# Performance work log

Hardware: AMD Instinct MI355X
Metric: run time of the kernel (lower is better)

## Reference

```python
import jax, jax.numpy as jnp
import numpy as np

# --- GridEncoder config (matches torch-ngp defaults) ---
D = 3                 # input_dim
L = 16                # num_levels
C = 2                 # level_dim
H = 16                # base_resolution
PLS = 2.0             # per_level_scale
LOG2_HASHMAP = 19
MAX_PARAMS = 2 ** LOG2_HASHMAP
PRIMES = (1, 2654435761, 805459861)  # fast_hash primes for D=3
ALIGN_CORNERS = False


def _level_meta():
    """Replicates the offsets computation in GridEncoder.__init__ and the
    kernel's per-level resolution / hash-vs-dense decision."""
    metas = []
    off = 0
    for l in range(L):
        res = int(np.ceil(H * PLS ** l))            # kernel: ceil(exp2(l*S)*H - 1) + 1 == H*2^l here
        full = (res if ALIGN_CORNERS else res + 1) ** D
        params = min(MAX_PARAMS, full)
        params = int(np.ceil(params / 8) * 8)       # pad to multiple of 8
        hashed = full > params                      # kernel: stride > hashmap_size after index loop
        metas.append((off, params, res, hashed))
        off += params
    return metas, off

METAS, TOTAL_PARAMS = _level_meta()


def setup_inputs() -> dict:
    key = jax.random.key(0)
    k1, k2 = jax.random.split(key)
    B = 1048576
    inputs = jax.random.uniform(k1, (B, D), dtype=jnp.float32, minval=-1.0, maxval=1.0)
    # reset_parameters(): uniform(-1e-4, 1e-4)
    embeddings = jax.random.uniform(k2, (TOTAL_PARAMS, C), dtype=jnp.float32,
                                    minval=-1e-4, maxval=1e-4)
    return {"inputs": inputs, "embeddings": embeddings}


def _grid_encode(x, embeddings):
    """x: [B, D] in [0, 1]. Returns [B, L*C]."""
    corner_bits = jnp.array([[(c >> d) & 1 for d in range(D)] for c in range(2 ** D)],
                            dtype=jnp.uint32)                       # [8, D]
    primes = jnp.array(PRIMES, dtype=jnp.uint32)
    outs = []
    for l, (off, size, res, hashed) in enumerate(METAS):
        scale = float(np.exp2(l) * H - 1.0)                          # exp2(l*S)*H - 1, S = log2(2) = 1
        pos = x * scale + (0.0 if ALIGN_CORNERS else 0.5)            # [B, D]
        pg_f = jnp.floor(pos)
        frac = pos - pg_f                                            # [B, D] linear interp weights
        pg = pg_f.astype(jnp.uint32)                                 # [B, D]
        corners = pg[None, :, :] + corner_bits[:, None, :]           # [8, B, D]
        # N-linear interpolation weights: prod over dims of frac / (1-frac)
        w = jnp.prod(jnp.where(corner_bits[:, None, :] == 1,
                               frac[None, :, :], 1.0 - frac[None, :, :]), axis=-1)  # [8, B]
        if hashed:
            # fast_hash: xor of pos_grid[d] * primes[d] in wrapping uint32
            idx = corners[..., 0] * primes[0]
            for d in range(1, D):
                idx = idx ^ (corners[..., d] * primes[d])
        else:
            base = res if ALIGN_CORNERS else res + 1
            stride = jnp.array([base ** d for d in range(D)], dtype=jnp.uint32)
            idx = (corners * stride).sum(axis=-1).astype(jnp.uint32)
        idx = (idx % jnp.uint32(size)) + jnp.uint32(off)             # [8, B]
        emb = embeddings[idx]                                        # [8, B, C] gather
        outs.append(jnp.einsum('kb,kbc->bc', w, emb))                # [B, C]
    return jnp.concatenate(outs, axis=-1)                            # [B, L*C], level-major


def reference(inputs, embeddings):
    bound = 1.0
    x = (inputs + bound) / (2.0 * bound)   # map to [0, 1]
    return _grid_encode(x, embeddings)
```

## Files before the change

kernel.cpp:

```cpp
#include <hip/hip_runtime.h>
#include <cstdint>


namespace {

using f32x2 = __attribute__((ext_vector_type(2))) float;
using f32x4 = __attribute__((ext_vector_type(4))) float;

__device__ __forceinline__ void level_setup(
    float x, float y, float z, uint32_t l,
    uint32_t idx[8], float w[8]) {
  uint32_t res = 16u << l;
  float scale = (float)res - 1.0f;

  float px = x * scale + 0.5f;
  float py = y * scale + 0.5f;
  float pz = z * scale + 0.5f;
  float gx = floorf(px), gy = floorf(py), gz = floorf(pz);
  float rx = px - gx, ry = py - gy, rz = pz - gz;
  uint32_t ix = (uint32_t)gx, iy = (uint32_t)gy, iz = (uint32_t)gz;

  uint32_t off = (l >= 3u) ? (l * 524288u - 1257368u)
                           : ((l == 0u) ? 0u : ((l == 1u) ? 4920u : 40864u));
  bool hashed = (l >= 3u);

  uint32_t base = res + 1u;
  uint32_t bb = base * base;
  const uint32_t P2 = 2654435761u, P3 = 805459861u;

  uint32_t dy0 = iy * base, dy1 = dy0 + base;
  uint32_t dz0 = iz * bb,   dz1 = dz0 + bb;
  uint32_t hy0 = iy * P2,   hy1 = hy0 + P2;
  uint32_t hz0 = iz * P3,   hz1 = hz0 + P3;

#pragma unroll
  for (int c = 0; c < 8; ++c) {
    uint32_t cx = ix + (uint32_t)(c & 1);
    uint32_t h = (cx ^ ((c & 2) ? hy1 : hy0) ^ ((c & 4) ? hz1 : hz0)) & 0x7FFFFu;
    uint32_t d = cx + ((c & 2) ? dy1 : dy0) + ((c & 4) ? dz1 : dz0);
    idx[c] = (hashed ? h : d) + off;
  }

  float wx1 = rx, wx0 = 1.0f - rx;
  float wy1 = ry, wy0 = 1.0f - ry;
  float wz1 = rz, wz0 = 1.0f - rz;
#pragma unroll
  for (int c = 0; c < 8; ++c) {
    w[c] = ((c & 1) ? wx1 : wx0) *
           ((c & 2) ? wy1 : wy0) *
           ((c & 4) ? wz1 : wz0);
  }
}

__global__ __launch_bounds__(256) void gather_lm_kernel(
    const float* __restrict__ in,
    const f32x2* __restrict__ emb,
    f32x2* __restrict__ ws,
    uint32_t B) {
  uint32_t l = blockIdx.y;
  uint32_t p = blockIdx.x * 256u + threadIdx.x;
  if (p >= B) return;

  float x = (__builtin_nontemporal_load(&in[p * 3 + 0]) + 1.0f) * 0.5f;
  float y = (__builtin_nontemporal_load(&in[p * 3 + 1]) + 1.0f) * 0.5f;
  float z = (__builtin_nontemporal_load(&in[p * 3 + 2]) + 1.0f) * 0.5f;

  uint32_t idx[8];
  float w[8];
  level_setup(x, y, z, l, idx, w);

  f32x2 e[8];
#pragma unroll
  for (int c = 0; c < 8; ++c) e[c] = emb[idx[c]];

  float o0 = 0.0f, o1 = 0.0f;
#pragma unroll
  for (int c = 0; c < 8; ++c) {
    o0 = fmaf(w[c], e[c].x, o0);
    o1 = fmaf(w[c], e[c].y, o1);
  }

  f32x2 r; r.x = o0; r.y = o1;
  __builtin_nontemporal_store(r, &ws[(size_t)l * B + p]);
}

__global__ __launch_bounds__(256) void transpose_kernel(
    const f32x2* __restrict__ ws,
    f32x4* __restrict__ out,
    uint32_t B) {
  __shared__ f32x2 lds[16 * 257];
  uint32_t tid = threadIdx.x;
  uint32_t p0 = blockIdx.x * 256u;

#pragma unroll
  for (uint32_t l = 0; l < 16u; ++l) {
    lds[l * 257u + tid] =
        __builtin_nontemporal_load(&ws[(size_t)l * B + p0 + tid]);
  }
  __syncthreads();

#pragma unroll
  for (uint32_t m = 0; m < 8u; ++m) {
    uint32_t lin = m * 256u + tid;
    uint32_t q = lin >> 3;
    uint32_t j2 = lin & 7u;
    f32x2 a = lds[(2u * j2)      * 257u + q];
    f32x2 b = lds[(2u * j2 + 1u) * 257u + q];
    f32x4 v; v.x = a.x; v.y = a.y; v.z = b.x; v.w = b.y;
    __builtin_nontemporal_store(v, &out[(size_t)p0 * 8u + lin]);
  }
}

__global__ __launch_bounds__(256) void grid_encode_fallback(
    const float* __restrict__ in, const f32x2* __restrict__ emb,
    f32x4* __restrict__ out, uint32_t B) {
  uint32_t p = blockIdx.x * 256u + threadIdx.x;
  if (p >= B) return;
  float x = (in[p * 3 + 0] + 1.0f) * 0.5f;
  float y = (in[p * 3 + 1] + 1.0f) * 0.5f;
  float z = (in[p * 3 + 2] + 1.0f) * 0.5f;
#pragma unroll 1
  for (uint32_t l = 0; l < 16u; l += 2u) {
    uint32_t ia[8], ib[8]; float wa[8], wb[8];
    level_setup(x, y, z, l, ia, wa);
    level_setup(x, y, z, l + 1u, ib, wb);
    f32x2 ea[8], eb[8];
#pragma unroll
    for (int c = 0; c < 8; ++c) ea[c] = emb[ia[c]];
#pragma unroll
    for (int c = 0; c < 8; ++c) eb[c] = emb[ib[c]];
    float a0 = 0, a1 = 0, b0 = 0, b1 = 0;
#pragma unroll
    for (int c = 0; c < 8; ++c) {
      a0 = fmaf(wa[c], ea[c].x, a0);
      a1 = fmaf(wa[c], ea[c].y, a1);
      b0 = fmaf(wb[c], eb[c].x, b0);
      b1 = fmaf(wb[c], eb[c].y, b1);
    }
    f32x4 v; v.x = a0; v.y = a1; v.z = b0; v.w = b1;
    out[(size_t)p * 8u + (l >> 1)] = v;
  }
}

}

extern "C" void kernel_launch(void* const* d_in, const int* in_sizes, int n_in,
                              void* d_out, int out_size, void* d_ws, size_t ws_size,
                              hipStream_t stream) {
  (void)n_in; (void)out_size;
  const float* in = (const float*)d_in[0];
  const f32x2* emb = (const f32x2*)d_in[1];
  f32x4* out = (f32x4*)d_out;
  uint32_t B = (uint32_t)(in_sizes[0] / 3);
  uint32_t pblocks = (B + 255u) / 256u;

  size_t ws_needed = (size_t)16 * B * sizeof(f32x2);
  if (ws_size >= ws_needed) {
    f32x2* ws = (f32x2*)d_ws;
    hipLaunchKernelGGL(gather_lm_kernel, dim3(pblocks, 16), dim3(256), 0,
                       stream, in, emb, ws, B);
    hipLaunchKernelGGL(transpose_kernel, dim3(pblocks), dim3(256), 0,
                       stream, ws, out, B);
  } else {
    hipLaunchKernelGGL(grid_encode_fallback, dim3(pblocks), dim3(256), 0,
                       stream, in, emb, out, B);
  }
}
```

Before: 619.4 us.

## Pair hashed x-neighbour gathers into 16-byte loads and simplify transpose

In the gather kernel, hashed levels with even ix now fetch both x-neighbours with one aligned 16-byte load, because ix^h and (ix+1)^h differ only in the low bit, then pick the halves by parity. Dense and hashed levels are split into separate branches, which avoids computing both index forms. The transpose kernel drops its LDS staging and has each thread read two level-major pairs and write one 16-byte output. This cuts the number of random memory transactions in the gather, but adds branch divergence on ix parity, and the transpose now reads the workspace with a stride pattern that may coalesce less well.

```diff
diff --git a/kernel.cpp b/kernel.cpp
--- a/kernel.cpp
+++ b/kernel.cpp
@@ -65,19 +65,71 @@
   float y = (__builtin_nontemporal_load(&in[p * 3 + 1]) + 1.0f) * 0.5f;
   float z = (__builtin_nontemporal_load(&in[p * 3 + 2]) + 1.0f) * 0.5f;
 
-  uint32_t idx[8];
-  float w[8];
-  level_setup(x, y, z, l, idx, w);
+  uint32_t res = 16u << l;
+  float scale = (float)res - 1.0f;
+  float px = x * scale + 0.5f;
+  float py = y * scale + 0.5f;
+  float pz = z * scale + 0.5f;
+  float gx = floorf(px), gy = floorf(py), gz = floorf(pz);
+  float rx = px - gx, ry = py - gy, rz = pz - gz;
+  uint32_t ix = (uint32_t)gx, iy = (uint32_t)gy, iz = (uint32_t)gz;
 
   f32x2 e[8];
-#pragma unroll
-  for (int c = 0; c < 8; ++c) e[c] = emb[idx[c]];
+
+  if (l >= 3u) {
+    uint32_t off = l * 524288u - 1257368u;
+    const f32x2* __restrict__ tab = emb + off;
+    const uint32_t P2 = 2654435761u, P3 = 805459861u;
+    uint32_t hy0 = iy * P2, hy1 = hy0 + P2;
+    uint32_t hz0 = iz * P3, hz1 = hz0 + P3;
+    uint32_t hb0 = hy0 ^ hz0, hb1 = hy1 ^ hz0, hb2 = hy0 ^ hz1, hb3 = hy1 ^ hz1;
+    uint32_t hb[4] = {hb0, hb1, hb2, hb3};
+
+    if ((ix & 1u) == 0u) {
+#pragma unroll
+      for (int j = 0; j < 4; ++j) {
+        uint32_t h0 = (ix ^ hb[j]) & 0x7FFFFu;
+        f32x4 v = *reinterpret_cast<const f32x4*>(tab + (h0 & ~1u));
+        f32x2 lo; lo.x = v.x; lo.y = v.y;
+        f32x2 hi; hi.x = v.z; hi.y = v.w;
+        bool swap = (h0 & 1u) != 0u;
+        e[2 * j]     = swap ? hi : lo;
+        e[2 * j + 1] = swap ? lo : hi;
+      }
+    } else {
+      uint32_t ix1 = ix + 1u;
+#pragma unroll
+      for (int j = 0; j < 4; ++j) {
+        e[2 * j]     = tab[(ix  ^ hb[j]) & 0x7FFFFu];
+        e[2 * j + 1] = tab[(ix1 ^ hb[j]) & 0x7FFFFu];
+      }
+    }
+  } else {
+    uint32_t off = (l == 0u) ? 0u : ((l == 1u) ? 4920u : 40864u);
+    uint32_t base = res + 1u;
+    uint32_t bb = base * base;
+    uint32_t dy0 = iy * base, dy1 = dy0 + base;
+    uint32_t dz0 = iz * bb,   dz1 = dz0 + bb;
+#pragma unroll
+    for (int c = 0; c < 8; ++c) {
+      uint32_t cx = ix + (uint32_t)(c & 1);
+      uint32_t d = cx + ((c & 2) ? dy1 : dy0) + ((c & 4) ? dz1 : dz0);
+      e[c] = emb[d + off];
+    }
+  }
+
+  float wx1 = rx, wx0 = 1.0f - rx;
+  float wy1 = ry, wy0 = 1.0f - ry;
+  float wz1 = rz, wz0 = 1.0f - rz;
 
   float o0 = 0.0f, o1 = 0.0f;
 #pragma unroll
   for (int c = 0; c < 8; ++c) {
-    o0 = fmaf(w[c], e[c].x, o0);
-    o1 = fmaf(w[c], e[c].y, o1);
+    float w = ((c & 1) ? wx1 : wx0) *
+              ((c & 2) ? wy1 : wy0) *
+              ((c & 4) ? wz1 : wz0);
+    o0 = fmaf(w, e[c].x, o0);
+    o1 = fmaf(w, e[c].y, o1);
   }
 
   f32x2 r; r.x = o0; r.y = o1;
@@ -88,27 +140,14 @@
     const f32x2* __restrict__ ws,
     f32x4* __restrict__ out,
     uint32_t B) {
-  __shared__ f32x2 lds[16 * 257];
-  uint32_t tid = threadIdx.x;
-  uint32_t p0 = blockIdx.x * 256u;
-
-#pragma unroll
-  for (uint32_t l = 0; l < 16u; ++l) {
-    lds[l * 257u + tid] =
-        __builtin_nontemporal_load(&ws[(size_t)l * B + p0 + tid]);
-  }
-  __syncthreads();
-
-#pragma unroll
-  for (uint32_t m = 0; m < 8u; ++m) {
-    uint32_t lin = m * 256u + tid;
-    uint32_t q = lin >> 3;
-    uint32_t j2 = lin & 7u;
-    f32x2 a = lds[(2u * j2)      * 257u + q];
-    f32x2 b = lds[(2u * j2 + 1u) * 257u + q];
-    f32x4 v; v.x = a.x; v.y = a.y; v.z = b.x; v.w = b.y;
-    __builtin_nontemporal_store(v, &out[(size_t)p0 * 8u + lin]);
-  }
+  uint32_t t = blockIdx.x * 256u + threadIdx.x;
+  if (t >= B * 8u) return;
+  uint32_t j = t & 7u;
+  uint32_t q = t >> 3;
+  f32x2 a = __builtin_nontemporal_load(&ws[(size_t)(2u * j)      * B + q]);
+  f32x2 b = __builtin_nontemporal_load(&ws[(size_t)(2u * j + 1u) * B + q]);
+  f32x4 v; v.x = a.x; v.y = a.y; v.z = b.x; v.w = b.y;
+  __builtin_nontemporal_store(v, &out[t]);
 }
 
 __global__ __launch_bounds__(256) void grid_encode_fallback(
@@ -159,7 +198,8 @@
     f32x2* ws = (f32x2*)d_ws;
     hipLaunchKernelGGL(gather_lm_kernel, dim3(pblocks, 16), dim3(256), 0,
                        stream, in, emb, ws, B);
-    hipLaunchKernelGGL(transpose_kernel, dim3(pblocks), dim3(256), 0,
+    uint32_t tblocks = (B * 8u + 255u) / 256u;
+    hipLaunchKernelGGL(transpose_kernel, dim3(tblocks), dim3(256), 0,
                        stream, ws, out, B);
   } else {
     hipLaunchKernelGGL(grid_encode_fallback, dim3(pblocks), dim3(256), 0,
```

Measured after the change: 608.6 us. Within noise of the previous version (-1.7%).

## Fuse level-major gather and transpose into one persistent software-pipelined kernel

Applied to the files above, without the earlier changes.

Replaces the two-kernel scheme (per-level gather into a workspace, then an LDS transpose) with one persistent kernel. Each block loops over chunks of points, computes all 16 levels per point, and overlaps gathers for the next level with interpolation of the current one. Results go into LDS and are written transposed straight to the output. This removes the workspace write and read round-trip through HBM and the second launch. The costs are less level-major locality for the embedding gathers (all levels touched by one block at once), higher register pressure from double-buffered gathers, and a fixed 1024-block grid.

```diff
diff --git a/kernel.cpp b/kernel.cpp
--- a/kernel.cpp
+++ b/kernel.cpp
@@ -7,12 +7,11 @@
 using f32x2 = __attribute__((ext_vector_type(2))) float;
 using f32x4 = __attribute__((ext_vector_type(4))) float;
 
-__device__ __forceinline__ void level_setup(
+__device__ __forceinline__ void level_setup_g(
     float x, float y, float z, uint32_t l,
-    uint32_t idx[8], float w[8]) {
+    uint32_t g[8], float f[6]) {
   uint32_t res = 16u << l;
   float scale = (float)res - 1.0f;
-
   float px = x * scale + 0.5f;
   float py = y * scale + 0.5f;
   float pz = z * scale + 0.5f;
@@ -20,125 +19,106 @@
   float rx = px - gx, ry = py - gy, rz = pz - gz;
   uint32_t ix = (uint32_t)gx, iy = (uint32_t)gy, iz = (uint32_t)gz;
 
-  uint32_t off = (l >= 3u) ? (l * 524288u - 1257368u)
-                           : ((l == 0u) ? 0u : ((l == 1u) ? 4920u : 40864u));
-  bool hashed = (l >= 3u);
-
-  uint32_t base = res + 1u;
-  uint32_t bb = base * base;
-  const uint32_t P2 = 2654435761u, P3 = 805459861u;
-
-  uint32_t dy0 = iy * base, dy1 = dy0 + base;
-  uint32_t dz0 = iz * bb,   dz1 = dz0 + bb;
-  uint32_t hy0 = iy * P2,   hy1 = hy0 + P2;
-  uint32_t hz0 = iz * P3,   hz1 = hz0 + P3;
-
+  if (l >= 3u) {
+    uint32_t off = l * 524288u - 1257368u;
+    const uint32_t P2 = 2654435761u, P3 = 805459861u;
+    uint32_t hy0 = iy * P2, hy1 = hy0 + P2;
+    uint32_t hz0 = iz * P3, hz1 = hz0 + P3;
+    uint32_t hb[4] = {hy0 ^ hz0, hy1 ^ hz0, hy0 ^ hz1, hy1 ^ hz1};
+    uint32_t ix1 = ix + 1u;
 #pragma unroll
-  for (int c = 0; c < 8; ++c) {
-    uint32_t cx = ix + (uint32_t)(c & 1);
-    uint32_t h = (cx ^ ((c & 2) ? hy1 : hy0) ^ ((c & 4) ? hz1 : hz0)) & 0x7FFFFu;
-    uint32_t d = cx + ((c & 2) ? dy1 : dy0) + ((c & 4) ? dz1 : dz0);
-    idx[c] = (hashed ? h : d) + off;
+    for (int j = 0; j < 4; ++j) {
+      g[2 * j]     = ((ix  ^ hb[j]) & 0x7FFFFu) + off;
+      g[2 * j + 1] = ((ix1 ^ hb[j]) & 0x7FFFFu) + off;
+    }
+  } else {
+    uint32_t off = (l == 0u) ? 0u : ((l == 1u) ? 4920u : 40864u);
+    uint32_t base = res + 1u;
+    uint32_t bb = base * base;
+    uint32_t dy0 = iy * base, dy1 = dy0 + base;
+    uint32_t dz0 = iz * bb,   dz1 = dz0 + bb;
+#pragma unroll
+    for (int c = 0; c < 8; ++c) {
+      g[c] = ix + (uint32_t)(c & 1) +
+             ((c & 2) ? dy1 : dy0) + ((c & 4) ? dz1 : dz0) + off;
+    }
   }
-
-  float wx1 = rx, wx0 = 1.0f - rx;
-  float wy1 = ry, wy0 = 1.0f - ry;
-  float wz1 = rz, wz0 = 1.0f - rz;
-#pragma unroll
-  for (int c = 0; c < 8; ++c) {
-    w[c] = ((c & 1) ? wx1 : wx0) *
-           ((c & 2) ? wy1 : wy0) *
-           ((c & 4) ? wz1 : wz0);
-  }
+  f[0] = 1.0f - rx; f[1] = rx;
+  f[2] = 1.0f - ry; f[3] = ry;
+  f[4] = 1.0f - rz; f[5] = rz;
 }
 
-__global__ __launch_bounds__(256) void gather_lm_kernel(
-    const float* __restrict__ in,
-    const f32x2* __restrict__ emb,
-    f32x2* __restrict__ ws,
-    uint32_t B) {
-  uint32_t l = blockIdx.y;
-  uint32_t p = blockIdx.x * 256u + threadIdx.x;
-  if (p >= B) return;
-
-  float x = (__builtin_nontemporal_load(&in[p * 3 + 0]) + 1.0f) * 0.5f;
-  float y = (__builtin_nontemporal_load(&in[p * 3 + 1]) + 1.0f) * 0.5f;
-  float z = (__builtin_nontemporal_load(&in[p * 3 + 2]) + 1.0f) * 0.5f;
-
-  uint32_t idx[8];
-  float w[8];
-  level_setup(x, y, z, l, idx, w);
-
-  f32x2 e[8];
-#pragma unroll
-  for (int c = 0; c < 8; ++c) e[c] = emb[idx[c]];
-
+__device__ __forceinline__ f32x2 interp8(const f32x2 e[8], const float f[6]) {
   float o0 = 0.0f, o1 = 0.0f;
 #pragma unroll
   for (int c = 0; c < 8; ++c) {
-    o0 = fmaf(w[c], e[c].x, o0);
-    o1 = fmaf(w[c], e[c].y, o1);
+    float w = f[c & 1] * f[2 + ((c >> 1) & 1)] * f[4 + ((c >> 2) & 1)];
+    o0 = fmaf(w, e[c].x, o0);
+    o1 = fmaf(w, e[c].y, o1);
   }
-
   f32x2 r; r.x = o0; r.y = o1;
-  __builtin_nontemporal_store(r, &ws[(size_t)l * B + p]);
+  return r;
 }
 
-__global__ __launch_bounds__(256) void transpose_kernel(
-    const f32x2* __restrict__ ws,
+__global__ __launch_bounds__(256, 4) void grid_encode_mono(
+    const float* __restrict__ in,
+    const f32x2* __restrict__ emb,
     f32x4* __restrict__ out,
-    uint32_t B) {
+    uint32_t B, uint32_t sweep, uint32_t nchunk) {
   __shared__ f32x2 lds[16 * 257];
   uint32_t tid = threadIdx.x;
-  uint32_t p0 = blockIdx.x * 256u;
+
+  for (uint32_t c = 0; c < nchunk; ++c) {
+    uint32_t cb = c * sweep + blockIdx.x * 256u;
+    uint32_t p = cb + tid;
+    uint32_t pc = (p < B) ? p : (B - 1u);
+
+    float x = (__builtin_nontemporal_load(&in[pc * 3 + 0]) + 1.0f) * 0.5f;
+    float y = (__builtin_nontemporal_load(&in[pc * 3 + 1]) + 1.0f) * 0.5f;
+    float z = (__builtin_nontemporal_load(&in[pc * 3 + 2]) + 1.0f) * 0.5f;
+
+    uint32_t gA[8]; float fA[6];
+    level_setup_g(x, y, z, 0u, gA, fA);
+    f32x2 eA[8];
+#pragma unroll
+    for (int k = 0; k < 8; ++k) eA[k] = emb[gA[k]];
+
+#pragma unroll 1
+    for (uint32_t lp = 0; lp < 8u; ++lp) {
+      uint32_t l0 = 2u * lp, l1 = l0 + 1u;
+
+      uint32_t gB[8]; float fB[6];
+      level_setup_g(x, y, z, l1, gB, fB);
+      f32x2 eB[8];
+#pragma unroll
+      for (int k = 0; k < 8; ++k) eB[k] = emb[gB[k]];
+
+      lds[l0 * 257u + tid] = interp8(eA, fA);
+
+      if (lp < 7u) {
+        level_setup_g(x, y, z, l0 + 2u, gA, fA);
+#pragma unroll
+        for (int k = 0; k < 8; ++k) eA[k] = emb[gA[k]];
+      }
+
+      lds[l1 * 257u + tid] = interp8(eB, fB);
+    }
+
+    __syncthreads();
 
 #pragma unroll
-  for (uint32_t l = 0; l < 16u; ++l) {
-    lds[l * 257u + tid] =
-        __builtin_nontemporal_load(&ws[(size_t)l * B + p0 + tid]);
-  }
-  __syncthreads();
+    for (uint32_t m = 0; m < 8u; ++m) {
+      uint32_t lin = m * 256u + tid;
+      uint32_t q = lin >> 3, j = lin & 7u;
+      if (cb + q < B) {
+        f32x2 a = lds[(2u * j)      * 257u + q];
+        f32x2 b = lds[(2u * j + 1u) * 257u + q];
+        f32x4 v = {a.x, a.y, b.x, b.y};
+        __builtin_nontemporal_store(v, &out[(size_t)(cb + q) * 8u + j]);
+      }
+    }
 
-#pragma unroll
-  for (uint32_t m = 0; m < 8u; ++m) {
-    uint32_t lin = m * 256u + tid;
-    uint32_t q = lin >> 3;
-    uint32_t j2 = lin & 7u;
-    f32x2 a = lds[(2u * j2)      * 257u + q];
-    f32x2 b = lds[(2u * j2 + 1u) * 257u + q];
-    f32x4 v; v.x = a.x; v.y = a.y; v.z = b.x; v.w = b.y;
-    __builtin_nontemporal_store(v, &out[(size_t)p0 * 8u + lin]);
-  }
-}
-
-__global__ __launch_bounds__(256) void grid_encode_fallback(
-    const float* __restrict__ in, const f32x2* __restrict__ emb,
-    f32x4* __restrict__ out, uint32_t B) {
-  uint32_t p = blockIdx.x * 256u + threadIdx.x;
-  if (p >= B) return;
-  float x = (in[p * 3 + 0] + 1.0f) * 0.5f;
-  float y = (in[p * 3 + 1] + 1.0f) * 0.5f;
-  float z = (in[p * 3 + 2] + 1.0f) * 0.5f;
-#pragma unroll 1
-  for (uint32_t l = 0; l < 16u; l += 2u) {
-    uint32_t ia[8], ib[8]; float wa[8], wb[8];
-    level_setup(x, y, z, l, ia, wa);
-    level_setup(x, y, z, l + 1u, ib, wb);
-    f32x2 ea[8], eb[8];
-#pragma unroll
-    for (int c = 0; c < 8; ++c) ea[c] = emb[ia[c]];
-#pragma unroll
-    for (int c = 0; c < 8; ++c) eb[c] = emb[ib[c]];
-    float a0 = 0, a1 = 0, b0 = 0, b1 = 0;
-#pragma unroll
-    for (int c = 0; c < 8; ++c) {
-      a0 = fmaf(wa[c], ea[c].x, a0);
-      a1 = fmaf(wa[c], ea[c].y, a1);
-      b0 = fmaf(wb[c], eb[c].x, b0);
-      b1 = fmaf(wb[c], eb[c].y, b1);
-    }
-    f32x4 v; v.x = a0; v.y = a1; v.z = b0; v.w = b1;
-    out[(size_t)p * 8u + (l >> 1)] = v;
+    __syncthreads();
   }
 }
 
@@ -147,22 +127,17 @@
 extern "C" void kernel_launch(void* const* d_in, const int* in_sizes, int n_in,
                               void* d_out, int out_size, void* d_ws, size_t ws_size,
                               hipStream_t stream) {
-  (void)n_in; (void)out_size;
+  (void)n_in; (void)out_size; (void)d_ws; (void)ws_size;
   const float* in = (const float*)d_in[0];
   const f32x2* emb = (const f32x2*)d_in[1];
   f32x4* out = (f32x4*)d_out;
   uint32_t B = (uint32_t)(in_sizes[0] / 3);
+
   uint32_t pblocks = (B + 255u) / 256u;
+  uint32_t grid = pblocks < 1024u ? pblocks : 1024u;
+  uint32_t sweep = grid * 256u;
+  uint32_t nchunk = (B + sweep - 1u) / sweep;
 
-  size_t ws_needed = (size_t)16 * B * sizeof(f32x2);
-  if (ws_size >= ws_needed) {
-    f32x2* ws = (f32x2*)d_ws;
-    hipLaunchKernelGGL(gather_lm_kernel, dim3(pblocks, 16), dim3(256), 0,
-                       stream, in, emb, ws, B);
-    hipLaunchKernelGGL(transpose_kernel, dim3(pblocks), dim3(256), 0,
-                       stream, ws, out, B);
-  } else {
-    hipLaunchKernelGGL(grid_encode_fallback, dim3(pblocks), dim3(256), 0,
-                       stream, in, emb, out, B);
-  }
+  hipLaunchKernelGGL(grid_encode_mono, dim3(grid), dim3(256), 0, stream,
+                     in, emb, out, B, sweep, nchunk);
 }
```

After: 949.3 us. 53.3% more time.
